# Optimization experiments

Hardware: AMD Instinct MI355X
Metric: run time of the kernel (lower is better)

Reference implementation:

```python
import jax, jax.numpy as jnp
import numpy as np

VOXEL_SIZE = np.array([0.1, 0.05, 0.05], dtype=np.float32)  # (z, y, x)
COOR_OFFSET = np.array([-3.0, -40.0, 0.0], dtype=np.float32)  # (z, y, x)
KERNEL, PAD = 3, 1


def setup_inputs() -> dict:
    key = jax.random.key(0)
    ks = jax.random.split(key, 12)
    B, N, Cv, Cr, H, W = 4, 40000, 16, 32, 376, 1248
    # sparse voxel coords: (batch, z, y, x) on the KITTI 40x1600x1408 grid
    bidx = jax.random.randint(ks[0], (N, 1), 0, B)
    z = jax.random.randint(ks[1], (N, 1), 0, 40)
    y = jax.random.randint(ks[2], (N, 1), 0, 1600)
    x = jax.random.randint(ks[3], (N, 1), 0, 1408)
    voxel_coords = jnp.concatenate([bidx, z, y, x], axis=1).astype(jnp.int32)
    voxel_features = jax.random.normal(ks[4], (N, Cv), jnp.float32)
    rgb_features = jax.random.normal(ks[5], (B, Cr, H, W), jnp.float32)
    # KITTI-like calibration: P2 intrinsics, Trv2c lidar->cam, rect ~ I
    fu, fv, cu, cv = 720.0, 720.0, W / 2.0, H / 2.0
    P2_base = jnp.array([[fu, 0.0, cu, 44.9], [0.0, fv, cv, 0.1], [0.0, 0.0, 1.0, 0.003]], jnp.float32)
    P2 = jnp.tile(P2_base[None], (B, 1, 1)) + 0.01 * jax.random.normal(ks[6], (B, 3, 4), jnp.float32)
    T_base = jnp.array([[0.0, -1.0, 0.0, 0.0], [0.0, 0.0, -1.0, -0.08], [1.0, 0.0, 0.0, -0.27], [0.0, 0.0, 0.0, 1.0]], jnp.float32)
    Trv2c = jnp.tile(T_base[None], (B, 1, 1)) + 0.001 * jax.random.normal(ks[7], (B, 4, 4), jnp.float32)
    rect = jnp.tile(jnp.eye(4, dtype=jnp.float32)[None], (B, 1, 1)) + 0.001 * jax.random.normal(ks[8], (B, 4, 4), jnp.float32)
    rgb_coor_refine = 0.5 * jax.random.normal(ks[9], (B, 2), jnp.float32)
    dummy_batch_list = jnp.arange(B, dtype=jnp.int32)
    return {"voxel_features": voxel_features, "rgb_features": rgb_features, "P2": P2,
            "Trv2c": Trv2c, "rect": rect, "rgb_coor_refine": rgb_coor_refine,
            "voxel_coords": voxel_coords, "dummy_batch_list": dummy_batch_list}


def _fuse(voxel_features, rgb_features, P2, Trv2c, rect, rgb_coor_refine, voxel_coords, dummy_batch_list):
    B, Cr, H, W = rgb_features.shape
    N, Cv = voxel_features.shape
    # per-batch gather as in the torch forward's dummy lists
    rgb = rgb_features[dummy_batch_list]            # [B, Cr, H, W]
    P2d = P2[dummy_batch_list]                      # [B, 3, 4]
    Md = jnp.einsum('bij,bjk->bik', rect[dummy_batch_list], Trv2c[dummy_batch_list])  # [B,4,4]
    prd = rgb_coor_refine[dummy_batch_list]         # [B, 2]
    # simple sparse-tensor expansion: dilate each voxel to its kernel^3 neighborhood
    r = jnp.arange(-PAD, KERNEL - PAD)
    off = jnp.stack(jnp.meshgrid(r, r, r, indexing='ij'), axis=-1).reshape(-1, 3)  # [K3,3]
    K3 = off.shape[0]
    zyx = (voxel_coords[:, None, 1:] + off[None]).reshape(-1, 3)  # [M,3]
    b = jnp.broadcast_to(voxel_coords[:, 0:1], (N, K3)).reshape(-1)  # [M]
    M = zyx.shape[0]
    # voxel center in lidar frame: zyx -> xyz
    ctr_zyx = (zyx.astype(jnp.float32) + 0.5) * jnp.asarray(VOXEL_SIZE) + jnp.asarray(COOR_OFFSET)
    xyz1 = jnp.concatenate([ctr_zyx[:, ::-1], jnp.ones((M, 1), jnp.float32)], axis=1)  # [M,4]
    cam = jnp.einsum('mij,mj->mi', Md[b], xyz1)      # [M,4] camera frame
    img = jnp.einsum('mij,mj->mi', P2d[b], cam)      # [M,3] homogeneous pixels
    depth = img[:, 2]
    d = jnp.maximum(depth, 1e-3)
    u = img[:, 0] / d + prd[b, 0]
    v = img[:, 1] / d + prd[b, 1]
    valid = (depth > 1e-3) & (u >= 0) & (u <= W - 1) & (v >= 0) & (v <= H - 1)
    uc = jnp.clip(u, 0.0, W - 1.0)
    vc = jnp.clip(v, 0.0, H - 1.0)
    x0 = jnp.floor(uc).astype(jnp.int32); y0 = jnp.floor(vc).astype(jnp.int32)
    x1 = jnp.minimum(x0 + 1, W - 1);      y1 = jnp.minimum(y0 + 1, H - 1)
    wx = (uc - x0.astype(jnp.float32))[:, None]
    wy = (vc - y0.astype(jnp.float32))[:, None]
    f00 = rgb[b, :, y0, x0]; f10 = rgb[b, :, y0, x1]
    f01 = rgb[b, :, y1, x0]; f11 = rgb[b, :, y1, x1]
    samp = (f00 * (1 - wx) * (1 - wy) + f10 * wx * (1 - wy)
            + f01 * (1 - wx) * wy + f11 * wx * wy)
    samp = samp * valid[:, None].astype(samp.dtype)  # zero features outside image
    vf = jnp.broadcast_to(voxel_features[:, None, :], (N, K3, Cv)).reshape(M, Cv)
    return jnp.concatenate([vf, samp], axis=1)       # [M, Cv + Cr]


def reference(voxel_features, rgb_features, P2, Trv2c, rect, rgb_coor_refine, voxel_coords, dummy_batch_list):
    return _fuse(voxel_features, rgb_features, P2, Trv2c, rect, rgb_coor_refine, voxel_coords, dummy_batch_list)
```

## Files before the change

kernel.cpp:

```cpp
#include <hip/hip_runtime.h>

namespace {
constexpr int IMG_H = 376;
constexpr int IMG_W = 1248;
constexpr int HW = IMG_H * IMG_W;
constexpr int CV = 16;
constexpr int CR = 32;
constexpr int CO = CV + CR;
constexpr int K3 = 27;
constexpr int BLOCK = 256;
constexpr int LDSPAD = CO + 1;
typedef float floatx4 __attribute__((ext_vector_type(4)));
typedef float floatx2 __attribute__((ext_vector_type(2)));
typedef floatx2 __attribute__((aligned(4))) floatx2u;
}

__global__ void prep_kernel(const float* __restrict__ P2,
                            const float* __restrict__ Trv2c,
                            const float* __restrict__ rect,
                            const float* __restrict__ prd,
                            const int* __restrict__ dummy,
                            float* __restrict__ mats, int B) {
    int b = threadIdx.x;
    if (b >= B) return;
    int s = dummy[b];
    float* o = mats + b * 32;
    const float* R = rect + s * 16;
    const float* T = Trv2c + s * 16;
    for (int i = 0; i < 4; ++i) {
        for (int j = 0; j < 4; ++j) {
            float acc = R[i * 4 + 0] * T[0 * 4 + j];
            acc += R[i * 4 + 1] * T[1 * 4 + j];
            acc += R[i * 4 + 2] * T[2 * 4 + j];
            acc += R[i * 4 + 3] * T[3 * 4 + j];
            o[i * 4 + j] = acc;
        }
    }
    for (int i = 0; i < 12; ++i) o[16 + i] = P2[s * 12 + i];
    o[28] = prd[s * 2 + 0];
    o[29] = prd[s * 2 + 1];
}

__global__ __launch_bounds__(BLOCK) void fuse_kernel(
        const float* __restrict__ vfeat,
        const float* __restrict__ rgb,
        const float* __restrict__ mats,
        const int* __restrict__ vcoords,
        float* __restrict__ out,
        int N) {
    const int M = N * K3;
    __shared__ float lds[4][16][LDSPAD];

    const int t = threadIdx.x;
    const int wave = t >> 6;
    const int lane = t & 63;
    const int waveBase = blockIdx.x * BLOCK + wave * 64;
    const int m = waveBase + lane;
    const bool inR = (m < M);

    float s[CO];
    #pragma unroll
    for (int c = 0; c < CO; ++c) s[c] = 0.0f;

    if (inR) {
        int n = m / K3;
        int kk = m - n * K3;
        int4 vc = ((const int4*)vcoords)[n];
        int b = vc.x;
        int dz = kk / 9;
        int rem = kk - dz * 9;
        int dy = rem / 3;
        int dx = rem - dy * 3;

        float fz = ((float)(vc.y + dz - 1) + 0.5f) * 0.1f - 3.0f;
        float fy = ((float)(vc.z + dy - 1) + 0.5f) * 0.05f - 40.0f;
        float fx = ((float)(vc.w + dx - 1) + 0.5f) * 0.05f;

        const float* Mb = mats + b * 32;
        float cam0 = Mb[0]  * fx + Mb[1]  * fy + Mb[2]  * fz + Mb[3];
        float cam1 = Mb[4]  * fx + Mb[5]  * fy + Mb[6]  * fz + Mb[7];
        float cam2 = Mb[8]  * fx + Mb[9]  * fy + Mb[10] * fz + Mb[11];
        float cam3 = Mb[12] * fx + Mb[13] * fy + Mb[14] * fz + Mb[15];

        float img0 = Mb[16] * cam0 + Mb[17] * cam1 + Mb[18] * cam2 + Mb[19] * cam3;
        float img1 = Mb[20] * cam0 + Mb[21] * cam1 + Mb[22] * cam2 + Mb[23] * cam3;
        float img2 = Mb[24] * cam0 + Mb[25] * cam1 + Mb[26] * cam2 + Mb[27] * cam3;

        float depth = img2;
        float d = fmaxf(depth, 0.001f);
        float u = img0 / d + Mb[28];
        float v = img1 / d + Mb[29];

        bool valid = (depth > 0.001f) && (u >= 0.0f) && (u <= (float)(IMG_W - 1))
                     && (v >= 0.0f) && (v <= (float)(IMG_H - 1));

        const float4* vp4 = (const float4*)(vfeat + (size_t)n * CV);
        float4 vf0 = vp4[0], vf1 = vp4[1], vf2 = vp4[2], vf3 = vp4[3];
        s[0] = vf0.x;  s[1] = vf0.y;  s[2]  = vf0.z;  s[3]  = vf0.w;
        s[4] = vf1.x;  s[5] = vf1.y;  s[6]  = vf1.z;  s[7]  = vf1.w;
        s[8] = vf2.x;  s[9] = vf2.y;  s[10] = vf2.z;  s[11] = vf2.w;
        s[12] = vf3.x; s[13] = vf3.y; s[14] = vf3.z;  s[15] = vf3.w;

        if (valid) {
            int x0 = min((int)floorf(u), IMG_W - 2);
            int y0 = min((int)floorf(v), IMG_H - 2);
            float wx = u - (float)x0;
            float wy = v - (float)y0;
            float w00 = (1.0f - wx) * (1.0f - wy);
            float w10 = wx * (1.0f - wy);
            float w01 = (1.0f - wx) * wy;
            float w11 = wx * wy;
            const float* tap = rgb + (size_t)b * CR * HW + (size_t)y0 * IMG_W + x0;
            #pragma unroll
            for (int g = 0; g < 4; ++g) {
                floatx2 r0[8], r1[8];
                #pragma unroll
                for (int c = 0; c < 8; ++c) {
                    const float* p = tap + (size_t)(g * 8 + c) * HW;
                    r0[c] = *(const floatx2u*)p;
                    r1[c] = *(const floatx2u*)(p + IMG_W);
                }
                __builtin_amdgcn_sched_group_barrier(0x020, 16, 0);
                #pragma unroll
                for (int c = 0; c < 8; ++c) {
                    s[CV + g * 8 + c] = r0[c].x * w00 + r0[c].y * w10
                                      + r1[c].x * w01 + r1[c].y * w11;
                }
                __builtin_amdgcn_sched_group_barrier(0x002, 32, 0);
            }
        }
    }

    const size_t total = (size_t)M * CO;
    #pragma unroll 1
    for (int j = 0; j < 4; ++j) {
        __builtin_amdgcn_wave_barrier();
        if ((lane >> 4) == j && inR) {
            int r = lane & 15;
            #pragma unroll
            for (int c = 0; c < CO; ++c) lds[wave][r][c] = s[c];
        }
        __builtin_amdgcn_wave_barrier();
        size_t chunkBase = ((size_t)waveBase + (size_t)j * 16) * CO;
        #pragma unroll
        for (int i = 0; i < 3; ++i) {
            int g = i * 64 + lane;
            int row = g / 12;
            int c4 = (g - row * 12) * 4;
            floatx4 val;
            val.x = lds[wave][row][c4 + 0];
            val.y = lds[wave][row][c4 + 1];
            val.z = lds[wave][row][c4 + 2];
            val.w = lds[wave][row][c4 + 3];
            size_t idx = chunkBase + (size_t)g * 4;
            if (idx < total) {
                __builtin_nontemporal_store(val, (floatx4*)(out + idx));
            }
        }
        __builtin_amdgcn_wave_barrier();
    }
}

extern "C" void kernel_launch(void* const* d_in, const int* in_sizes, int n_in,
                              void* d_out, int out_size, void* d_ws, size_t ws_size,
                              hipStream_t stream) {
    const float* vfeat  = (const float*)d_in[0];
    const float* rgb    = (const float*)d_in[1];
    const float* P2     = (const float*)d_in[2];
    const float* Trv2c  = (const float*)d_in[3];
    const float* rect   = (const float*)d_in[4];
    const float* prd    = (const float*)d_in[5];
    const int* vcoords  = (const int*)d_in[6];
    const int* dummy    = (const int*)d_in[7];
    float* out = (float*)d_out;

    int B = in_sizes[7];
    int N = in_sizes[6] / 4;
    float* mats = (float*)d_ws;

    prep_kernel<<<1, 64, 0, stream>>>(P2, Trv2c, rect, prd, dummy, mats, B);

    int M = N * K3;
    int blocks = (M + BLOCK - 1) / BLOCK;
    fuse_kernel<<<blocks, BLOCK, 0, stream>>>(vfeat, rgb, mats, vcoords, out, N);
}
```

Baseline: 134.1 us.

## Split RGB channel sampling across lane pairs and load voxel features at store time

Each output row is now handled by two lanes, each sampling 16 of the 32 RGB channels, so a block covers 128 rows instead of 256. Voxel features are no longer held in registers. They are read straight from global memory, using voxel indices kept in shared memory, as the output is written. Launch bounds now request higher occupancy. The goal is fewer registers and more memory-level parallelism for the scattered bilinear gathers, at the cost of duplicating the projection math across each lane pair and launching twice as many blocks.

```diff
diff --git a/kernel.cpp b/kernel.cpp
--- a/kernel.cpp
+++ b/kernel.cpp
@@ -9,6 +9,7 @@
 constexpr int CO = CV + CR;
 constexpr int K3 = 27;
 constexpr int BLOCK = 256;
+constexpr int RPB = 128;
 constexpr int LDSPAD = CO + 1;
 typedef float floatx4 __attribute__((ext_vector_type(4)));
 typedef float floatx2 __attribute__((ext_vector_type(2)));
@@ -41,7 +42,7 @@
     o[29] = prd[s * 2 + 1];
 }
 
-__global__ __launch_bounds__(BLOCK) void fuse_kernel(
+__global__ __launch_bounds__(BLOCK, 8) void fuse_kernel(
         const float* __restrict__ vfeat,
         const float* __restrict__ rgb,
         const float* __restrict__ mats,
@@ -50,21 +51,25 @@
         int N) {
     const int M = N * K3;
     __shared__ float lds[4][16][LDSPAD];
+    __shared__ int   sn[4][32];
 
     const int t = threadIdx.x;
     const int wave = t >> 6;
     const int lane = t & 63;
-    const int waveBase = blockIdx.x * BLOCK + wave * 64;
-    const int m = waveBase + lane;
+    const int rl = lane >> 1;
+    const int h = lane & 1;
+    const int waveRow0 = blockIdx.x * RPB + wave * 32;
+    const int m = waveRow0 + rl;
     const bool inR = (m < M);
 
-    float s[CO];
+    float s[CV];
     #pragma unroll
-    for (int c = 0; c < CO; ++c) s[c] = 0.0f;
+    for (int c = 0; c < CV; ++c) s[c] = 0.0f;
 
     if (inR) {
         int n = m / K3;
         int kk = m - n * K3;
+        if (h == 0) sn[wave][rl] = n;
         int4 vc = ((const int4*)vcoords)[n];
         int b = vc.x;
         int dz = kk / 9;
@@ -94,13 +99,6 @@
         bool valid = (depth > 0.001f) && (u >= 0.0f) && (u <= (float)(IMG_W - 1))
                      && (v >= 0.0f) && (v <= (float)(IMG_H - 1));
 
-        const float4* vp4 = (const float4*)(vfeat + (size_t)n * CV);
-        float4 vf0 = vp4[0], vf1 = vp4[1], vf2 = vp4[2], vf3 = vp4[3];
-        s[0] = vf0.x;  s[1] = vf0.y;  s[2]  = vf0.z;  s[3]  = vf0.w;
-        s[4] = vf1.x;  s[5] = vf1.y;  s[6]  = vf1.z;  s[7]  = vf1.w;
-        s[8] = vf2.x;  s[9] = vf2.y;  s[10] = vf2.z;  s[11] = vf2.w;
-        s[12] = vf3.x; s[13] = vf3.y; s[14] = vf3.z;  s[15] = vf3.w;
-
         if (valid) {
             int x0 = min((int)floorf(u), IMG_W - 2);
             int y0 = min((int)floorf(v), IMG_H - 2);
@@ -110,50 +108,60 @@
             float w10 = wx * (1.0f - wy);
             float w01 = (1.0f - wx) * wy;
             float w11 = wx * wy;
-            const float* tap = rgb + (size_t)b * CR * HW + (size_t)y0 * IMG_W + x0;
+            const float* tap = rgb + (size_t)b * CR * HW
+                             + (size_t)h * CV * HW
+                             + (size_t)y0 * IMG_W + x0;
             #pragma unroll
-            for (int g = 0; g < 4; ++g) {
+            for (int g2 = 0; g2 < 2; ++g2) {
                 floatx2 r0[8], r1[8];
                 #pragma unroll
                 for (int c = 0; c < 8; ++c) {
-                    const float* p = tap + (size_t)(g * 8 + c) * HW;
+                    const float* p = tap + (size_t)(g2 * 8 + c) * HW;
                     r0[c] = *(const floatx2u*)p;
                     r1[c] = *(const floatx2u*)(p + IMG_W);
                 }
                 __builtin_amdgcn_sched_group_barrier(0x020, 16, 0);
                 #pragma unroll
                 for (int c = 0; c < 8; ++c) {
-                    s[CV + g * 8 + c] = r0[c].x * w00 + r0[c].y * w10
-                                      + r1[c].x * w01 + r1[c].y * w11;
+                    s[g2 * 8 + c] = r0[c].x * w00 + r0[c].y * w10
+                                  + r1[c].x * w01 + r1[c].y * w11;
                 }
-                __builtin_amdgcn_sched_group_barrier(0x002, 32, 0);
             }
         }
     }
 
     const size_t total = (size_t)M * CO;
+    const floatx4* vf4 = (const floatx4*)vfeat;
     #pragma unroll 1
-    for (int j = 0; j < 4; ++j) {
+    for (int j = 0; j < 2; ++j) {
         __builtin_amdgcn_wave_barrier();
-        if ((lane >> 4) == j && inR) {
-            int r = lane & 15;
+        if ((rl >> 4) == j && inR) {
+            int r = rl & 15;
             #pragma unroll
-            for (int c = 0; c < CO; ++c) lds[wave][r][c] = s[c];
+            for (int q = 0; q < 4; ++q) {
+                *(floatx4*)&lds[wave][r][CV + CV * h + 4 * q] =
+                    *(const floatx4*)&s[4 * q];
+            }
         }
         __builtin_amdgcn_wave_barrier();
-        size_t chunkBase = ((size_t)waveBase + (size_t)j * 16) * CO;
+        size_t chunkBase = ((size_t)waveRow0 + (size_t)j * 16) * CO;
         #pragma unroll
         for (int i = 0; i < 3; ++i) {
             int g = i * 64 + lane;
             int row = g / 12;
-            int c4 = (g - row * 12) * 4;
-            floatx4 val;
-            val.x = lds[wave][row][c4 + 0];
-            val.y = lds[wave][row][c4 + 1];
-            val.z = lds[wave][row][c4 + 2];
-            val.w = lds[wave][row][c4 + 3];
+            int c4 = g - row * 12;
             size_t idx = chunkBase + (size_t)g * 4;
             if (idx < total) {
+                floatx4 val;
+                if (c4 < 4) {
+                    val = vf4[(size_t)sn[wave][j * 16 + row] * 4 + c4];
+                } else {
+                    int cc = c4 * 4;
+                    val.x = lds[wave][row][cc + 0];
+                    val.y = lds[wave][row][cc + 1];
+                    val.z = lds[wave][row][cc + 2];
+                    val.w = lds[wave][row][cc + 3];
+                }
                 __builtin_nontemporal_store(val, (floatx4*)(out + idx));
             }
         }
@@ -181,6 +189,6 @@
     prep_kernel<<<1, 64, 0, stream>>>(P2, Trv2c, rect, prd, dummy, mats, B);
 
     int M = N * K3;
-    int blocks = (M + BLOCK - 1) / BLOCK;
+    int blocks = (M + RPB - 1) / RPB;
     fuse_kernel<<<blocks, BLOCK, 0, stream>>>(vfeat, rgb, mats, vcoords, out, N);
 }
```

New measurement: 173.4 us. +29.4%, slower.
